# Performance work log

Hardware: AMD Instinct MI355X
Metric: run time of the kernel (lower is better)

The kernel has to match this reference:

```python
import jax, jax.numpy as jnp
import numpy as np

DIM = 2048
N_HEADS = 16
Q_LORA = 1536
KV_LORA = 512
NOPE = 128
ROPE = 64
QK_HD = NOPE + ROPE  # 192
V_HD = 128
BS, SEQ = 2, 2048
EPS = 1e-6


def rmsnorm(x, w):
    var = jnp.mean(jnp.square(x), axis=-1, keepdims=True)
    return x * jax.lax.rsqrt(var + EPS) * w


def rope_cos_sin(seq_len, dim, dtype):
    inv_freq = 1.0 / (10000.0 ** (jnp.arange(0, dim, 2, dtype=jnp.float32) / dim))
    t = jnp.arange(seq_len, dtype=jnp.float32)
    freqs = jnp.outer(t, inv_freq)            # [S, dim/2]
    emb = jnp.concatenate([freqs, freqs], -1)  # [S, dim]
    return jnp.cos(emb).astype(dtype), jnp.sin(emb).astype(dtype)


def rotate_half(x):
    x1, x2 = jnp.split(x, 2, axis=-1)
    return jnp.concatenate([-x2, x1], axis=-1)


def apply_rope(x, cos, sin):
    # x: [B, S, H, D]; cos/sin: [S, D] -> broadcast over B, H
    return x * cos[None, :, None, :] + rotate_half(x) * sin[None, :, None, :]


def setup_inputs() -> dict:
    key = jax.random.key(0)
    ks = jax.random.split(key, 8)
    s = 0.02
    return {
        "x": jax.random.normal(ks[0], (BS, SEQ, DIM), jnp.float32),
        "wq_a_w": jax.random.normal(ks[1], (Q_LORA, DIM), jnp.float32) * s,
        "wq_a_b": jnp.zeros((Q_LORA,), jnp.float32),
        "q_norm_w": jnp.ones((Q_LORA,), jnp.float32),
        "wq_b_w": jax.random.normal(ks[2], (N_HEADS * QK_HD, Q_LORA), jnp.float32) * s,
        "wq_b_b": jnp.zeros((N_HEADS * QK_HD,), jnp.float32),
        "wkv_a_w": jax.random.normal(ks[3], (KV_LORA + ROPE, DIM), jnp.float32) * s,
        "wkv_a_b": jnp.zeros((KV_LORA + ROPE,), jnp.float32),
        "kv_norm_w": jnp.ones((KV_LORA,), jnp.float32),
        "wkv_b_w": jax.random.normal(ks[4], (N_HEADS * (NOPE + V_HD), KV_LORA), jnp.float32) * s,
        "wkv_b_b": jnp.zeros((N_HEADS * (NOPE + V_HD),), jnp.float32),
        "wo_w": jax.random.normal(ks[5], (DIM, N_HEADS * V_HD), jnp.float32) * s,
        "wo_b": jnp.zeros((DIM,), jnp.float32),
    }


def reference(x, wq_a_w, wq_a_b, q_norm_w, wq_b_w, wq_b_b,
              wkv_a_w, wkv_a_b, kv_norm_w, wkv_b_w, wkv_b_b, wo_w, wo_b):
    bs, seq_len, _ = x.shape
    # Q path: low-rank down, RMSNorm, up
    q = x @ wq_a_w.T + wq_a_b
    q = rmsnorm(q, q_norm_w)
    q = q @ wq_b_w.T + wq_b_b
    q = q.reshape(bs, seq_len, N_HEADS, QK_HD)
    q_nope, q_pe = q[..., :NOPE], q[..., NOPE:]
    # KV path: joint low-rank + decoupled rope key
    kv = x @ wkv_a_w.T + wkv_a_b
    kv_c, k_pe = kv[..., :KV_LORA], kv[..., KV_LORA:]
    k_pe = k_pe[:, :, None, :]  # [B, S, 1, ROPE]
    cos, sin = rope_cos_sin(seq_len, ROPE, x.dtype)
    q_pe = apply_rope(q_pe, cos, sin)
    k_pe = apply_rope(k_pe, cos, sin)
    # naive mode: materialize per-head K/V
    kv_c = rmsnorm(kv_c, kv_norm_w)
    kvb = (kv_c @ wkv_b_w.T + wkv_b_b).reshape(bs, seq_len, N_HEADS, NOPE + V_HD)
    k_nope, v = kvb[..., :NOPE], kvb[..., NOPE:]
    q_full = jnp.concatenate([q_nope, q_pe], axis=-1)            # [B,S,H,192]
    k_full = jnp.concatenate(
        [k_nope, jnp.broadcast_to(k_pe, (bs, seq_len, N_HEADS, ROPE))], axis=-1)
    scale = 1.0 / np.sqrt(QK_HD)
    scores = jnp.einsum('bqhd,bkhd->bhqk', q_full, k_full) * scale
    causal = jnp.tril(jnp.ones((seq_len, seq_len), bool))
    scores = jnp.where(causal[None, None], scores, jnp.finfo(scores.dtype).min)
    attn = jax.nn.softmax(scores, axis=-1)
    out = jnp.einsum('bhqk,bkhd->bqhd', attn, v)
    out = out.reshape(bs, seq_len, N_HEADS * V_HD)
    return out @ wo_w.T + wo_b
```

## Files before the change

kernel.cpp:

```cpp
#include <hip/hip_runtime.h>

#define SEQ 2048
#define NHEADS 16

typedef __bf16 bf16;
typedef __bf16 bf16x8 __attribute__((ext_vector_type(8)));
typedef __bf16 bf16x4v __attribute__((ext_vector_type(4)));
typedef float f32x4 __attribute__((ext_vector_type(4)));
typedef unsigned short u16x4 __attribute__((ext_vector_type(4)));
typedef unsigned short u16x8 __attribute__((ext_vector_type(8)));

static __device__ __forceinline__ float bf2f(unsigned short u) {
    union { unsigned u32; float f; } v; v.u32 = ((unsigned)u) << 16; return v.f;
}
static __device__ __forceinline__ unsigned short f2bf(float f) {
    union { float f; unsigned u; } v; v.f = f;
    unsigned u = v.u;
    unsigned r = u + 0x7fffu + ((u >> 16) & 1u);
    return (unsigned short)(r >> 16);
}

static __device__ __forceinline__ void g2l16(const unsigned short* g, unsigned short* l) {
    __builtin_amdgcn_global_load_lds(
        (const __attribute__((address_space(1))) unsigned int*)(unsigned long long)g,
        (__attribute__((address_space(3))) unsigned int*)(unsigned int)(unsigned long long)l,
        16, 0, 0);
}

static __device__ __forceinline__ int xcd_swz(int id, int n) {
    int q = n >> 3, r = n & 7;
    int x = id & 7, o = id >> 3;
    return (x < r ? x * (q + 1) : r * (q + 1) + (x - r) * q) + o;
}

__global__ void detect_dtype(const unsigned* __restrict__ qnw, int* __restrict__ flag) {
    if (threadIdx.x == 0 && blockIdx.x == 0)
        *flag = (qnw[0] == 0x3F800000u) ? 1 : 0;
}

struct CvtArgs {
    const void* src[13];
    unsigned short* dst[13];
    int n[13];
    int startblk[14];
};
__global__ __launch_bounds__(256) void to_bf16_all(CvtArgs a, const int* __restrict__ flag) {
    int bx = blockIdx.x;
    int t = 0;
    while (bx >= a.startblk[t + 1]) ++t;
    int base = (bx - a.startblk[t]) * 4096;
    int n = a.n[t];
    int hi = base + 4096; if (hi > n) hi = n;
    int cnt = hi - base;
    if (*flag) {
        const f32x4* s = (const f32x4*)a.src[t] + (base >> 2);
        u16x4* d = (u16x4*)(a.dst[t] + base);
        int c4 = cnt >> 2;
        for (int e = threadIdx.x; e < c4; e += 256) {
            f32x4 v = s[e];
            u16x4 o;
#pragma unroll
            for (int j = 0; j < 4; ++j) o[j] = f2bf(v[j]);
            d[e] = o;
        }
    } else {
        const uint4* s = (const uint4*)a.src[t] + (base >> 3);
        uint4* d = (uint4*)(a.dst[t] + base);
        int c8 = cnt >> 3;
        for (int e = threadIdx.x; e < c8; e += 256) d[e] = s[e];
    }
}

struct GemmP {
    const unsigned short* A; int lda;
    const unsigned short* W;
    const unsigned short* bias;
    unsigned short* C; float* Cf; int ldc;
    int N; int K; const int* flagp;
    int nbx;
    float oscale;
};

static __device__ void gemm_body(const GemmP g, int bx, int by,
                                 unsigned short* Al, unsigned short* Bl)
{
    const int lane = threadIdx.x & 63;
    const int w    = threadIdx.x >> 6;
    const int r    = lane & 15;
    const int quad = lane >> 4;
    const int m0 = by << 7;
    const int n0 = bx << 7;
    const int wr = (w >> 1) << 6;
    const int wc = (w & 1) << 6;

    const int srow = lane >> 2;
    const int scol = (lane & 3) << 3;
    const int j0 = w * 2, j1 = w * 2 + 1;

    const unsigned short* a0 = g.A + (size_t)(m0 + j0 * 16 + srow) * g.lda + scol;
    const unsigned short* a1 = g.A + (size_t)(m0 + j1 * 16 + srow) * g.lda + scol;
    int bn0 = n0 + j0 * 16 + srow; if (bn0 >= g.N) bn0 = g.N - 1;
    int bn1 = n0 + j1 * 16 + srow; if (bn1 >= g.N) bn1 = g.N - 1;
    const unsigned short* b0 = g.W + (size_t)bn0 * g.K + scol;
    const unsigned short* b1 = g.W + (size_t)bn1 * g.K + scol;

    f32x4 acc[4][4];
#pragma unroll
    for (int mt = 0; mt < 4; ++mt)
#pragma unroll
        for (int nt = 0; nt < 4; ++nt) acc[mt][nt] = (f32x4){0.f, 0.f, 0.f, 0.f};

    auto stage = [&](int buf, int kb) {
        unsigned short* Ad = Al + (buf << 12);
        unsigned short* Bd = Bl + (buf << 12);
        g2l16(a0 + kb, &Ad[j0 * 512 + lane * 8]);
        g2l16(a1 + kb, &Ad[j1 * 512 + lane * 8]);
        g2l16(b0 + kb, &Bd[j0 * 512 + lane * 8]);
        g2l16(b1 + kb, &Bd[j1 * 512 + lane * 8]);
    };

    stage(0, 0);
    int cur = 0;
    const int nk = g.K >> 5;
#pragma unroll 1
    for (int t = 0; t < nk; ++t) {
        if (t + 1 < nk) {
            stage(cur ^ 1, (t + 1) << 5);
            asm volatile("s_waitcnt vmcnt(4)" ::: "memory");
        } else {
            asm volatile("s_waitcnt vmcnt(0)" ::: "memory");
        }
        __builtin_amdgcn_s_barrier();

        const unsigned short* As = Al + (cur << 12);
        const unsigned short* Bs = Bl + (cur << 12);
        bf16x8 af[4], bfr[4];
#pragma unroll
        for (int mt = 0; mt < 4; ++mt)
            af[mt] = *(const bf16x8*)&As[(wr + mt * 16 + r) * 32 + quad * 8];
#pragma unroll
        for (int nt = 0; nt < 4; ++nt)
            bfr[nt] = *(const bf16x8*)&Bs[(wc + nt * 16 + r) * 32 + quad * 8];
#pragma unroll
        for (int mt = 0; mt < 4; ++mt)
#pragma unroll
            for (int nt = 0; nt < 4; ++nt)
                acc[mt][nt] = __builtin_amdgcn_mfma_f32_16x16x32_bf16(af[mt], bfr[nt], acc[mt][nt], 0, 0, 0);

        asm volatile("s_waitcnt lgkmcnt(0)" ::: "memory");
        __builtin_amdgcn_s_barrier();
        cur ^= 1;
    }

    int outf = (g.Cf && g.flagp) ? *g.flagp : 0;
    float bv[4];
#pragma unroll
    for (int nt = 0; nt < 4; ++nt) {
        int col = n0 + wc + nt * 16 + r;
        bv[nt] = (g.bias && col < g.N) ? bf2f(g.bias[col]) : 0.f;
    }
#pragma unroll
    for (int mt = 0; mt < 4; ++mt) {
#pragma unroll
        for (int i = 0; i < 4; ++i) {
            int row = m0 + wr + mt * 16 + quad * 4 + i;
#pragma unroll
            for (int nt = 0; nt < 4; ++nt) {
                int col = n0 + wc + nt * 16 + r;
                if (col < g.N) {
                    float v = (acc[mt][nt][i] + bv[nt]) * g.oscale;
                    size_t idx = (size_t)row * g.ldc + col;
                    if (g.Cf) {
                        if (outf) g.Cf[idx] = v;
                        else      ((unsigned short*)g.Cf)[idx] = f2bf(v);
                    } else {
                        g.C[idx] = f2bf(v);
                    }
                }
            }
        }
    }
}

__global__ __launch_bounds__(256) void gemm_one(GemmP g) {
    __shared__ unsigned short Al[2 * 4096];
    __shared__ unsigned short Bl[2 * 4096];
    int id = xcd_swz(blockIdx.x, gridDim.x);
    gemm_body(g, id % g.nbx, id / g.nbx, Al, Bl);
}

__global__ __launch_bounds__(256) void gemm_two(GemmP g0, GemmP g1, int nblk0) {
    __shared__ unsigned short Al[2 * 4096];
    __shared__ unsigned short Bl[2 * 4096];
    int id = xcd_swz(blockIdx.x, gridDim.x);
    if (id < nblk0) {
        gemm_body(g0, id % g0.nbx, id / g0.nbx, Al, Bl);
    } else {
        id -= nblk0;
        gemm_body(g1, id % g1.nbx, id / g1.nbx, Al, Bl);
    }
}

__global__ __launch_bounds__(256) void rmsnorm_ip2(
    unsigned short* __restrict__ d0, int s0w, int w0w, const unsigned short* __restrict__ w0,
    unsigned short* __restrict__ d1, int s1w, int w1w, const unsigned short* __restrict__ w1,
    int rows0)
{
    __shared__ float red[256];
    int row = blockIdx.x;
    unsigned short* p; const unsigned short* wt; int stride, width;
    if (row < rows0) { p = d0; wt = w0; stride = s0w; width = w0w; }
    else { row -= rows0; p = d1; wt = w1; stride = s1w; width = w1w; }
    p += (size_t)row * stride;

    const int nv = width >> 3;
    u16x8* pv = (u16x8*)p;
    const u16x8* wv = (const u16x8*)wt;

    float ss = 0.f;
    for (int j = threadIdx.x; j < nv; j += 256) {
        u16x8 v = pv[j];
#pragma unroll
        for (int k = 0; k < 8; ++k) { float f = bf2f(v[k]); ss += f * f; }
    }
    red[threadIdx.x] = ss;
    __syncthreads();
    for (int s = 128; s > 0; s >>= 1) {
        if ((int)threadIdx.x < s) red[threadIdx.x] += red[threadIdx.x + s];
        __syncthreads();
    }
    float rstd = rsqrtf(red[0] / (float)width + 1e-6f);
    for (int j = threadIdx.x; j < nv; j += 256) {
        u16x8 v = pv[j], g = wv[j], o;
#pragma unroll
        for (int k = 0; k < 8; ++k) o[k] = f2bf(bf2f(v[k]) * rstd * bf2f(g[k]));
        pv[j] = o;
    }
}

__global__ __launch_bounds__(256) void rope_ip_all(
    unsigned short* __restrict__ qbuf, unsigned short* __restrict__ kvbf)
{
    __shared__ float cst[32], snt[32];
    int row = blockIdx.x;
    int s = row & (SEQ - 1);
    if (threadIdx.x < 32) {
        int i = threadIdx.x;
        float inv = exp2f(-(float)i * (13.2877123795f / 32.0f));
        float ang = (float)s * inv;
        cst[i] = cosf(ang); snt[i] = sinf(ang);
    }
    __syncthreads();
    for (int t = threadIdx.x; t < 544; t += 256) {
        int i = t & 31;
        float c = cst[i], sn = snt[i];
        unsigned short* p;
        if (t < 512) p = qbuf + (size_t)row * 3072 + (t >> 5) * 192 + 128;
        else         p = kvbf + (size_t)row * 576 + 512;
        float x1 = bf2f(p[i]), x2 = bf2f(p[i + 32]);
        p[i]      = f2bf(x1 * c - x2 * sn);
        p[i + 32] = f2bf(x2 * c + x1 * sn);
    }
}

__global__ __launch_bounds__(256) void mla_attn_mfma(
    const unsigned short* __restrict__ qbuf,
    const unsigned short* __restrict__ kvb,
    const unsigned short* __restrict__ kvbuf,
    unsigned short* __restrict__ attn_out)
{
    __shared__ unsigned short Kt[2][32 * 200];
    __shared__ unsigned short Vt[2][128 * 44];
    __shared__ unsigned short Pm[4][16 * 40];

    const int bh = blockIdx.y;
    const int b = bh >> 4, h = bh & 15;
    const int tid  = threadIdx.x;
    const int lane = tid & 63;
    const int w    = tid >> 6;
    const int r    = lane & 15;
    const int quad = lane >> 4;
    const int rowk0 = b * SEQ;

    int kldso[3];
    const unsigned short* ksrc[3];
    int krst[3];
#pragma unroll
    for (int j = 0; j < 3; ++j) {
        int v = tid + j * 256;
        int row = v / 24, c = v % 24;
        kldso[j] = row * 200 + c * 8;
        if (c < 16) { ksrc[j] = kvb + (size_t)(rowk0 + row) * 4096 + h * 256 + c * 8; krst[j] = 4096; }
        else        { ksrc[j] = kvbuf + (size_t)(rowk0 + row) * 576 + 512 + (c - 16) * 8; krst[j] = 576; }
    }
    const int vp  = tid & 15;
    const int vdc = tid >> 4;
    const unsigned short* vsrc = kvb + (size_t)(rowk0 + 2 * vp) * 4096 + h * 256 + 128 + vdc * 8;

    auto stageK = [&](int buf, const uint4& k0, const uint4& k1, const uint4& k2) {
        *(uint4*)&Kt[buf][kldso[0]] = k0;
        *(uint4*)&Kt[buf][kldso[1]] = k1;
        *(uint4*)&Kt[buf][kldso[2]] = k2;
    };
    auto stageV = [&](int buf, const uint4& va, const uint4& vb_) {
        const unsigned* ea = (const unsigned*)&va;
        const unsigned* eb = (const unsigned*)&vb_;
        unsigned short* Vd = &Vt[buf][0];
#pragma unroll
        for (int t = 0; t < 4; ++t) {
            unsigned pe = (ea[t] & 0xffffu) | (eb[t] << 16);
            unsigned po = (ea[t] >> 16) | (eb[t] & 0xffff0000u);
            *(unsigned*)&Vd[(vdc * 8 + 2 * t) * 44 + 2 * vp]     = pe;
            *(unsigned*)&Vd[(vdc * 8 + 2 * t + 1) * 44 + 2 * vp] = po;
        }
    };

    unsigned short* Pw = Pm[w];

#pragma unroll 1
    for (int half = 0; half < 2; ++half) {
        const int qt = half ? (31 - (int)blockIdx.x) : (int)blockIdx.x;
        const int qbase = qt * 64 + w * 16;
        const int nkb = 2 * qt + 2;
        const int itmax = 2 * qt + (w >> 1);

        bf16x8 qf[6];
        {
            const unsigned short* qp =
                qbuf + (size_t)(rowk0 + qbase + r) * 3072 + h * 192 + quad * 8;
#pragma unroll
            for (int t = 0; t < 6; ++t) qf[t] = *(const bf16x8*)(qp + t * 32);
        }

        f32x4 O[8];
#pragma unroll
        for (int f = 0; f < 8; ++f) O[f] = (f32x4){0.f, 0.f, 0.f, 0.f};
        float mi = -1e30f, li = 0.f;

        uint4 pk0, pk1, pk2, pv0, pv1;

        __syncthreads();
        pk0 = *(const uint4*)(ksrc[0]);
        pk1 = *(const uint4*)(ksrc[1]);
        pk2 = *(const uint4*)(ksrc[2]);
        pv0 = *(const uint4*)(vsrc);
        pv1 = *(const uint4*)(vsrc + 4096);
        stageK(0, pk0, pk1, pk2);
        stageV(0, pv0, pv1);
        __syncthreads();

#pragma unroll 1
        for (int it = 0; it < nkb; ++it) {
            const int p = it & 1;
            const int kb = it * 32;
            const bool more = (it + 1 < nkb);

            if (more) {
                const size_t koff = (size_t)(kb + 32);
                pk0 = *(const uint4*)(ksrc[0] + koff * krst[0]);
                pk1 = *(const uint4*)(ksrc[1] + koff * krst[1]);
                pk2 = *(const uint4*)(ksrc[2] + koff * krst[2]);
                pv0 = *(const uint4*)(vsrc + koff * 4096);
                pv1 = *(const uint4*)(vsrc + koff * 4096 + 4096);
            }

            if (it <= itmax) {
                f32x4 s0 = {0.f, 0.f, 0.f, 0.f}, s1 = {0.f, 0.f, 0.f, 0.f};
                __builtin_amdgcn_s_setprio(1);
#pragma unroll
                for (int t = 0; t < 6; ++t) {
                    bf16x8 k0 = *(const bf16x8*)&Kt[p][r * 200 + t * 32 + quad * 8];
                    bf16x8 k1 = *(const bf16x8*)&Kt[p][(16 + r) * 200 + t * 32 + quad * 8];
                    s0 = __builtin_amdgcn_mfma_f32_16x16x32_bf16(k0, qf[t], s0, 0, 0, 0);
                    s1 = __builtin_amdgcn_mfma_f32_16x16x32_bf16(k1, qf[t], s1, 0, 0, 0);
                }
                __builtin_amdgcn_s_setprio(0);

                const int qrow = qbase + r;
                float a0[4], a1[4];
                float mx = -1e30f;
                if (kb + 31 > qbase) {
#pragma unroll
                    for (int i = 0; i < 4; ++i) {
                        a0[i] = (kb + quad * 4 + i      <= qrow) ? s0[i] : -1e30f;
                        a1[i] = (kb + 16 + quad * 4 + i <= qrow) ? s1[i] : -1e30f;
                        mx = fmaxf(mx, fmaxf(a0[i], a1[i]));
                    }
                } else {
#pragma unroll
                    for (int i = 0; i < 4; ++i) {
                        a0[i] = s0[i];
                        a1[i] = s1[i];
                        mx = fmaxf(mx, fmaxf(a0[i], a1[i]));
                    }
                }
                mx = fmaxf(mx, __shfl_xor(mx, 16, 64));
                mx = fmaxf(mx, __shfl_xor(mx, 32, 64));

                if (!__all(mx <= mi + 8.f)) {
                    float mn = fmaxf(mi, mx);
                    float al = __expf(mi - mn);
#pragma unroll
                    for (int f = 0; f < 8; ++f) O[f] *= al;
                    li *= al;
                    mi = mn;
                }

                float p0[4], p1[4], ps = 0.f;
#pragma unroll
                for (int i = 0; i < 4; ++i) {
                    p0[i] = __expf(a0[i] - mi);
                    p1[i] = __expf(a1[i] - mi);
                    ps += p0[i] + p1[i];
                }
                ps += __shfl_xor(ps, 16, 64);
                ps += __shfl_xor(ps, 32, 64);
                li += ps;

                bf16x4v b0v, b1v;
#pragma unroll
                for (int i = 0; i < 4; ++i) {
                    b0v[i] = (__bf16)p0[i];
                    b1v[i] = (__bf16)p1[i];
                }
                *(bf16x4v*)&Pw[r * 40 + quad * 4]      = b0v;
                *(bf16x4v*)&Pw[r * 40 + 16 + quad * 4] = b1v;

                bf16x8 pf = *(const bf16x8*)&Pw[r * 40 + quad * 8];
                __builtin_amdgcn_s_setprio(1);
#pragma unroll
                for (int f = 0; f < 8; ++f) {
                    bf16x8 vb = *(const bf16x8*)&Vt[p][(f * 16 + r) * 44 + quad * 8];
                    O[f] = __builtin_amdgcn_mfma_f32_16x16x32_bf16(vb, pf, O[f], 0, 0, 0);
                }
                __builtin_amdgcn_s_setprio(0);
            }

            if (more) {
                const int q2 = 1 - p;
                stageK(q2, pk0, pk1, pk2);
                stageV(q2, pv0, pv1);
                __syncthreads();
            }
        }

        float inv = (li > 0.f) ? (1.f / li) : 0.f;
        unsigned short* orow = attn_out + (size_t)(rowk0 + qbase + r) * 2048 + h * 128;
#pragma unroll
        for (int f = 0; f < 8; ++f) {
            bf16x4v o;
#pragma unroll
            for (int i = 0; i < 4; ++i) o[i] = (__bf16)(O[f][i] * inv);
            *(bf16x4v*)&orow[f * 16 + quad * 4] = o;
        }
    }
}

extern "C" void kernel_launch(void* const* d_in, const int* in_sizes, int n_in,
                              void* d_out, int out_size, void* d_ws, size_t ws_size,
                              hipStream_t stream)
{
    char* ws = (char*)d_ws;
    size_t off = 0;
    auto alloc = [&](size_t bytes) -> void* {
        void* p = ws + off;
        off = (off + bytes + 255) & ~(size_t)255;
        return p;
    };

    int* flag = (int*)alloc(256);

    const int nx = 4096 * 2048;
    unsigned short* xb    = (unsigned short*)alloc((size_t)nx * 2);
    unsigned short* wqa   = (unsigned short*)alloc((size_t)1536 * 2048 * 2);
    unsigned short* wqab  = (unsigned short*)alloc(1536 * 2);
    unsigned short* qnw   = (unsigned short*)alloc(1536 * 2);
    unsigned short* wqb   = (unsigned short*)alloc((size_t)3072 * 1536 * 2);
    unsigned short* wqbb  = (unsigned short*)alloc(3072 * 2);
    unsigned short* wkva  = (unsigned short*)alloc((size_t)576 * 2048 * 2);
    unsigned short* wkvab = (unsigned short*)alloc(576 * 2);
    unsigned short* kvnw  = (unsigned short*)alloc(512 * 2);
    unsigned short* wkvb  = (unsigned short*)alloc((size_t)4096 * 512 * 2);
    unsigned short* wkvbb = (unsigned short*)alloc(4096 * 2);
    unsigned short* wo    = (unsigned short*)alloc((size_t)2048 * 2048 * 2);
    unsigned short* wob   = (unsigned short*)alloc(2048 * 2);

    unsigned short* qa   = (unsigned short*)alloc((size_t)4096 * 1536 * 2);
    unsigned short* qbuf = (unsigned short*)alloc((size_t)4096 * 3072 * 2);
    unsigned short* kvbf = (unsigned short*)alloc((size_t)4096 * 576 * 2);
    unsigned short* kvb  = (unsigned short*)alloc((size_t)4096 * 4096 * 2);
    unsigned short* attn = xb;

    const int M = 4096;
    dim3 blk(256);

    detect_dtype<<<dim3(1), dim3(64), 0, stream>>>((const unsigned*)d_in[3], flag);

    {
        CvtArgs a;
        unsigned short* dsts[13] = {xb, wqa, wqab, qnw, wqb, wqbb, wkva, wkvab, kvnw, wkvb, wkvbb, wo, wob};
        int pb = 0;
        for (int i = 0; i < 13; ++i) {
            a.src[i] = d_in[i];
            a.dst[i] = dsts[i];
            a.n[i] = in_sizes[i];
            a.startblk[i] = pb;
            pb += (in_sizes[i] + 4095) / 4096;
        }
        a.startblk[13] = pb;
        to_bf16_all<<<dim3(pb), blk, 0, stream>>>(a, flag);
    }

    auto mkg = [](const unsigned short* A, int lda, const unsigned short* W,
                  const unsigned short* bias, unsigned short* C, float* Cf, int ldc,
                  int N, int K, const int* fl, float osc) -> GemmP {
        GemmP g;
        g.A = A; g.lda = lda; g.W = W; g.bias = bias;
        g.C = C; g.Cf = Cf; g.ldc = ldc; g.N = N; g.K = K; g.flagp = fl;
        g.nbx = (N + 127) / 128;
        g.oscale = osc;
        return g;
    };

    {
        GemmP gqa  = mkg(xb, 2048, wqa,  wqab,  qa,   nullptr, 1536, 1536, 2048, nullptr, 1.f);
        GemmP gkva = mkg(xb, 2048, wkva, wkvab, kvbf, nullptr, 576,  576,  2048, nullptr, 1.f);
        int nb0 = gqa.nbx * (M / 128), nb1 = gkva.nbx * (M / 128);
        gemm_two<<<dim3(nb0 + nb1), blk, 0, stream>>>(gqa, gkva, nb0);
    }

    rmsnorm_ip2<<<dim3(2 * M), blk, 0, stream>>>(qa, 1536, 1536, qnw,
                                                 kvbf, 576, 512, kvnw, M);

    {
        GemmP gqb  = mkg(qa,   1536, wqb,  wqbb,  qbuf, nullptr, 3072, 3072, 1536, nullptr, 0.0721687836487f);
        GemmP gkvb = mkg(kvbf, 576,  wkvb, wkvbb, kvb,  nullptr, 4096, 4096, 512,  nullptr, 1.f);
        int nb0 = gqb.nbx * (M / 128), nb1 = gkvb.nbx * (M / 128);
        gemm_two<<<dim3(nb0 + nb1), blk, 0, stream>>>(gqb, gkvb, nb0);
    }

    rope_ip_all<<<dim3(M), blk, 0, stream>>>(qbuf, kvbf);

    mla_attn_mfma<<<dim3(16, 2 * NHEADS), blk, 0, stream>>>(qbuf, kvb, kvbf, attn);

    {
        GemmP gout = mkg(attn, 2048, wo, wob, nullptr, (float*)d_out, 2048, 2048, 2048, flag, 1.f);
        gemm_one<<<dim3(gout.nbx * (M / 128)), blk, 0, stream>>>(gout);
    }
}
```

Before: 491.8 us.

## Vectorize GEMM epilogue stores, drop XCD swizzle and hand-tuned waitcnt pipelining

Swaps the MFMA operand order so each lane holds four contiguous output columns. The epilogue can then load bias and store results as 4-wide vectors instead of scalar strided writes. It also removes the XCD-aware block remapping and goes back to plain blockIdx indexing with a 2D grid for the output projection. The explicit vmcnt/lgkmcnt waits are replaced by __syncthreads, which likely waits for all outstanding loads and weakens the overlap of loads with compute. Cache locality across XCDs may also suffer.

```diff
diff --git a/kernel.cpp b/kernel.cpp
--- a/kernel.cpp
+++ b/kernel.cpp
@@ -25,12 +25,6 @@
         (const __attribute__((address_space(1))) unsigned int*)(unsigned long long)g,
         (__attribute__((address_space(3))) unsigned int*)(unsigned int)(unsigned long long)l,
         16, 0, 0);
-}
-
-static __device__ __forceinline__ int xcd_swz(int id, int n) {
-    int q = n >> 3, r = n & 7;
-    int x = id & 7, o = id >> 3;
-    return (x < r ? x * (q + 1) : r * (q + 1) + (x - r) * q) + o;
 }
 
 __global__ void detect_dtype(const unsigned* __restrict__ qnw, int* __restrict__ flag) {
@@ -120,17 +114,10 @@
     };
 
     stage(0, 0);
+    __syncthreads();
     int cur = 0;
-    const int nk = g.K >> 5;
-#pragma unroll 1
-    for (int t = 0; t < nk; ++t) {
-        if (t + 1 < nk) {
-            stage(cur ^ 1, (t + 1) << 5);
-            asm volatile("s_waitcnt vmcnt(4)" ::: "memory");
-        } else {
-            asm volatile("s_waitcnt vmcnt(0)" ::: "memory");
-        }
-        __builtin_amdgcn_s_barrier();
+    for (int kb = 0; kb < g.K; kb += 32) {
+        if (kb + 32 < g.K) stage(cur ^ 1, kb + 32);
 
         const unsigned short* As = Al + (cur << 12);
         const unsigned short* Bs = Bl + (cur << 12);
@@ -145,37 +132,46 @@
         for (int mt = 0; mt < 4; ++mt)
 #pragma unroll
             for (int nt = 0; nt < 4; ++nt)
-                acc[mt][nt] = __builtin_amdgcn_mfma_f32_16x16x32_bf16(af[mt], bfr[nt], acc[mt][nt], 0, 0, 0);
-
-        asm volatile("s_waitcnt lgkmcnt(0)" ::: "memory");
-        __builtin_amdgcn_s_barrier();
+                acc[mt][nt] = __builtin_amdgcn_mfma_f32_16x16x32_bf16(bfr[nt], af[mt], acc[mt][nt], 0, 0, 0);
+
+        __syncthreads();
         cur ^= 1;
     }
 
     int outf = (g.Cf && g.flagp) ? *g.flagp : 0;
-    float bv[4];
-#pragma unroll
-    for (int nt = 0; nt < 4; ++nt) {
-        int col = n0 + wc + nt * 16 + r;
-        bv[nt] = (g.bias && col < g.N) ? bf2f(g.bias[col]) : 0.f;
-    }
 #pragma unroll
     for (int mt = 0; mt < 4; ++mt) {
-#pragma unroll
-        for (int i = 0; i < 4; ++i) {
-            int row = m0 + wr + mt * 16 + quad * 4 + i;
-#pragma unroll
-            for (int nt = 0; nt < 4; ++nt) {
-                int col = n0 + wc + nt * 16 + r;
-                if (col < g.N) {
-                    float v = (acc[mt][nt][i] + bv[nt]) * g.oscale;
-                    size_t idx = (size_t)row * g.ldc + col;
-                    if (g.Cf) {
-                        if (outf) g.Cf[idx] = v;
-                        else      ((unsigned short*)g.Cf)[idx] = f2bf(v);
+        size_t rb = (size_t)(m0 + wr + mt * 16 + r) * g.ldc;
+#pragma unroll
+        for (int nt = 0; nt < 4; ++nt) {
+            int col = n0 + wc + nt * 16 + quad * 4;
+            if (col < g.N) {
+                float v[4];
+#pragma unroll
+                for (int i = 0; i < 4; ++i) v[i] = acc[mt][nt][i];
+                if (g.bias) {
+                    u16x4 bb = *(const u16x4*)&g.bias[col];
+#pragma unroll
+                    for (int i = 0; i < 4; ++i) v[i] += bf2f(bb[i]);
+                }
+#pragma unroll
+                for (int i = 0; i < 4; ++i) v[i] *= g.oscale;
+                size_t idx = rb + col;
+                if (g.Cf) {
+                    if (outf) {
+                        f32x4 o = {v[0], v[1], v[2], v[3]};
+                        *(f32x4*)&g.Cf[idx] = o;
                     } else {
-                        g.C[idx] = f2bf(v);
+                        u16x4 o;
+#pragma unroll
+                        for (int i = 0; i < 4; ++i) o[i] = f2bf(v[i]);
+                        *(u16x4*)&((unsigned short*)g.Cf)[idx] = o;
                     }
+                } else {
+                    u16x4 o;
+#pragma unroll
+                    for (int i = 0; i < 4; ++i) o[i] = f2bf(v[i]);
+                    *(u16x4*)&g.C[idx] = o;
                 }
             }
         }
@@ -185,14 +181,13 @@
 __global__ __launch_bounds__(256) void gemm_one(GemmP g) {
     __shared__ unsigned short Al[2 * 4096];
     __shared__ unsigned short Bl[2 * 4096];
-    int id = xcd_swz(blockIdx.x, gridDim.x);
-    gemm_body(g, id % g.nbx, id / g.nbx, Al, Bl);
+    gemm_body(g, blockIdx.x, blockIdx.y, Al, Bl);
 }
 
 __global__ __launch_bounds__(256) void gemm_two(GemmP g0, GemmP g1, int nblk0) {
     __shared__ unsigned short Al[2 * 4096];
     __shared__ unsigned short Bl[2 * 4096];
-    int id = xcd_swz(blockIdx.x, gridDim.x);
+    int id = blockIdx.x;
     if (id < nblk0) {
         gemm_body(g0, id % g0.nbx, id / g0.nbx, Al, Bl);
     } else {
@@ -545,6 +540,6 @@
 
     {
         GemmP gout = mkg(attn, 2048, wo, wob, nullptr, (float*)d_out, 2048, 2048, 2048, flag, 1.f);
-        gemm_one<<<dim3(gout.nbx * (M / 128)), blk, 0, stream>>>(gout);
-    }
-}
+        gemm_one<<<dim3(gout.nbx, M / 128), blk, 0, stream>>>(gout);
+    }
+}
```

Measured after the change: 482.4 us. About the same (-1.9%).

## Fold log2e into Q scale, use exp2, simplify GEMM sync, drop XCD swizzle

Applied to the files above, without the earlier changes.

The Q output scale now includes the log2(e) factor, so softmax can use the native exp2 instruction in place of __expf, saving a multiply per exponent. The V tile row pitch shrinks from 44 to 40 elements, which may change LDS bank conflicts. The GEMM main loop goes back to plain __syncthreads around each step instead of explicit vmcnt waits and barriers, so loads are less tightly overlapped with MFMA work. XCD-aware block swizzling is removed, which may reduce L2 locality.

```diff
diff --git a/kernel.cpp b/kernel.cpp
--- a/kernel.cpp
+++ b/kernel.cpp
@@ -25,12 +25,6 @@
         (const __attribute__((address_space(1))) unsigned int*)(unsigned long long)g,
         (__attribute__((address_space(3))) unsigned int*)(unsigned int)(unsigned long long)l,
         16, 0, 0);
-}
-
-static __device__ __forceinline__ int xcd_swz(int id, int n) {
-    int q = n >> 3, r = n & 7;
-    int x = id & 7, o = id >> 3;
-    return (x < r ? x * (q + 1) : r * (q + 1) + (x - r) * q) + o;
 }
 
 __global__ void detect_dtype(const unsigned* __restrict__ qnw, int* __restrict__ flag) {
@@ -120,17 +114,10 @@
     };
 
     stage(0, 0);
+    __syncthreads();
     int cur = 0;
-    const int nk = g.K >> 5;
-#pragma unroll 1
-    for (int t = 0; t < nk; ++t) {
-        if (t + 1 < nk) {
-            stage(cur ^ 1, (t + 1) << 5);
-            asm volatile("s_waitcnt vmcnt(4)" ::: "memory");
-        } else {
-            asm volatile("s_waitcnt vmcnt(0)" ::: "memory");
-        }
-        __builtin_amdgcn_s_barrier();
+    for (int kb = 0; kb < g.K; kb += 32) {
+        if (kb + 32 < g.K) stage(cur ^ 1, kb + 32);
 
         const unsigned short* As = Al + (cur << 12);
         const unsigned short* Bs = Bl + (cur << 12);
@@ -147,8 +134,7 @@
             for (int nt = 0; nt < 4; ++nt)
                 acc[mt][nt] = __builtin_amdgcn_mfma_f32_16x16x32_bf16(af[mt], bfr[nt], acc[mt][nt], 0, 0, 0);
 
-        asm volatile("s_waitcnt lgkmcnt(0)" ::: "memory");
-        __builtin_amdgcn_s_barrier();
+        __syncthreads();
         cur ^= 1;
     }
 
@@ -185,14 +171,13 @@
 __global__ __launch_bounds__(256) void gemm_one(GemmP g) {
     __shared__ unsigned short Al[2 * 4096];
     __shared__ unsigned short Bl[2 * 4096];
-    int id = xcd_swz(blockIdx.x, gridDim.x);
-    gemm_body(g, id % g.nbx, id / g.nbx, Al, Bl);
+    gemm_body(g, blockIdx.x, blockIdx.y, Al, Bl);
 }
 
 __global__ __launch_bounds__(256) void gemm_two(GemmP g0, GemmP g1, int nblk0) {
     __shared__ unsigned short Al[2 * 4096];
     __shared__ unsigned short Bl[2 * 4096];
-    int id = xcd_swz(blockIdx.x, gridDim.x);
+    int id = blockIdx.x;
     if (id < nblk0) {
         gemm_body(g0, id % g0.nbx, id / g0.nbx, Al, Bl);
     } else {
@@ -270,7 +255,7 @@
     unsigned short* __restrict__ attn_out)
 {
     __shared__ unsigned short Kt[2][32 * 200];
-    __shared__ unsigned short Vt[2][128 * 44];
+    __shared__ unsigned short Vt[2][128 * 40];
     __shared__ unsigned short Pm[4][16 * 40];
 
     const int bh = blockIdx.y;
@@ -310,8 +295,8 @@
         for (int t = 0; t < 4; ++t) {
             unsigned pe = (ea[t] & 0xffffu) | (eb[t] << 16);
             unsigned po = (ea[t] >> 16) | (eb[t] & 0xffff0000u);
-            *(unsigned*)&Vd[(vdc * 8 + 2 * t) * 44 + 2 * vp]     = pe;
-            *(unsigned*)&Vd[(vdc * 8 + 2 * t + 1) * 44 + 2 * vp] = po;
+            *(unsigned*)&Vd[(vdc * 8 + 2 * t) * 40 + 2 * vp]     = pe;
+            *(unsigned*)&Vd[(vdc * 8 + 2 * t + 1) * 40 + 2 * vp] = po;
         }
     };
 
@@ -399,7 +384,7 @@
 
                 if (!__all(mx <= mi + 8.f)) {
                     float mn = fmaxf(mi, mx);
-                    float al = __expf(mi - mn);
+                    float al = __builtin_amdgcn_exp2f(mi - mn);
 #pragma unroll
                     for (int f = 0; f < 8; ++f) O[f] *= al;
                     li *= al;
@@ -409,8 +394,8 @@
                 float p0[4], p1[4], ps = 0.f;
 #pragma unroll
                 for (int i = 0; i < 4; ++i) {
-                    p0[i] = __expf(a0[i] - mi);
-                    p1[i] = __expf(a1[i] - mi);
+                    p0[i] = __builtin_amdgcn_exp2f(a0[i] - mi);
+                    p1[i] = __builtin_amdgcn_exp2f(a1[i] - mi);
                     ps += p0[i] + p1[i];
                 }
                 ps += __shfl_xor(ps, 16, 64);
@@ -430,7 +415,7 @@
                 __builtin_amdgcn_s_setprio(1);
 #pragma unroll
                 for (int f = 0; f < 8; ++f) {
-                    bf16x8 vb = *(const bf16x8*)&Vt[p][(f * 16 + r) * 44 + quad * 8];
+                    bf16x8 vb = *(const bf16x8*)&Vt[p][(f * 16 + r) * 40 + quad * 8];
                     O[f] = __builtin_amdgcn_mfma_f32_16x16x32_bf16(vb, pf, O[f], 0, 0, 0);
                 }
                 __builtin_amdgcn_s_setprio(0);
@@ -533,7 +518,7 @@
                                                  kvbf, 576, 512, kvnw, M);
 
     {
-        GemmP gqb  = mkg(qa,   1536, wqb,  wqbb,  qbuf, nullptr, 3072, 3072, 1536, nullptr, 0.0721687836487f);
+        GemmP gqb  = mkg(qa,   1536, wqb,  wqbb,  qbuf, nullptr, 3072, 3072, 1536, nullptr, 0.1041175648f);
         GemmP gkvb = mkg(kvbf, 576,  wkvb, wkvbb, kvb,  nullptr, 4096, 4096, 512,  nullptr, 1.f);
         int nb0 = gqb.nbx * (M / 128), nb1 = gkvb.nbx * (M / 128);
         gemm_two<<<dim3(nb0 + nb1), blk, 0, stream>>>(gqb, gkvb, nb0);
@@ -545,6 +530,6 @@
 
     {
         GemmP gout = mkg(attn, 2048, wo, wob, nullptr, (float*)d_out, 2048, 2048, 2048, flag, 1.f);
-        gemm_one<<<dim3(gout.nbx * (M / 128)), blk, 0, stream>>>(gout);
-    }
-}
+        gemm_one<<<dim3(gout.nbx, M / 128), blk, 0, stream>>>(gout);
+    }
+}
```

Result: faster. 455.2 us (-7.4%).
